# Kernel tuning notes

Measured on AMD Instinct MI355X. Metric: run time of the kernel, lower is better.

## Reference

```python
import jax, jax.numpy as jnp
import numpy as np

K_SIZE = 5


def extract_patches(x, k):
    # TF extract_image_patches with SAME zero padding, stride 1.
    # x: [B,H,W,C] -> [B,H,W,k*k,C], patch index ordered row-major over offsets.
    pad = k // 2
    B, H, W, C = x.shape
    xp = jnp.pad(x, ((0, 0), (pad, pad), (pad, pad), (0, 0)))
    slices = [xp[:, i:i + H, j:j + W, :] for i in range(k) for j in range(k)]
    return jnp.stack(slices, axis=3)  # [B,H,W,k*k,C]


def setup_inputs() -> dict:
    key = jax.random.key(0)
    k1, k2, k3, k4 = jax.random.split(key, 4)
    B, H, W, C, BIN = 4, 128, 128, 64, 64
    return {
        "main": jax.random.normal(k1, (B, H, W, C), jnp.float32),
        "main_value": jax.random.normal(k2, (B, H, W, BIN), jnp.float32),
        "ref": jax.random.normal(k3, (B, H, W, C), jnp.float32),
        "ref_value": jax.random.normal(k4, (B, H, W, BIN), jnp.float32),
    }


def reference(main, main_value, ref, ref_value):
    k = K_SIZE
    # local window keys: [B,H,W,k*k,C], then append main itself -> k*k+1 slots
    ref_stacked = extract_patches(ref, k)
    ref_main = jnp.concatenate([ref_stacked, main[:, :, :, None, :]], axis=-2)
    attn = jnp.einsum('bhwc,bhwkc->bhwk', main, ref_main)
    attn = jax.nn.softmax(attn, axis=-1)
    # values: [B,H,W,k*k+1,bin]
    ref_value_stacked = extract_patches(ref_value, k)
    ref_main_value = jnp.concatenate(
        [ref_value_stacked, main_value[:, :, :, None, :]], axis=-2)
    aggregation = jnp.einsum('bhwk,bhwki->bhwi', attn, ref_main_value)
    return aggregation
```

## Files before the change

### kernel.cpp

```cpp
#include <hip/hip_runtime.h>

#define BATCH 4
#define HH 128
#define WW 128
#define CC 64
#define PADR 2
#define NK 25
#define TH 8
#define TW 8
#define HALO 12
#define HPOS 144
#define LSTRIDE 68

__global__ __launch_bounds__(256) void local_attn_kernel(
    const float* __restrict__ main_,
    const float* __restrict__ main_value,
    const float* __restrict__ ref,
    const float* __restrict__ ref_value,
    float* __restrict__ out)
{
    __shared__ float buf[HPOS * LSTRIDE];

    const int t    = threadIdx.x;
    const int blk  = blockIdx.x;
    const int bx   = blk & 15;
    const int by   = (blk >> 4) & 15;
    const int b    = blk >> 8;

    const int lane = t & 63;
    const int wave = t >> 6;
    const int pxl  = lane >> 2;
    const int cg   = lane & 3;
    const int ly   = wave * 2 + (pxl >> 3);
    const int lx   = pxl & 7;
    const int gy   = by * TH + ly;
    const int gx   = bx * TW + lx;

    const size_t img_base = (size_t)b * HH * WW * CC;
    const size_t px_off   = img_base + ((size_t)gy * WW + gx) * CC + cg * 16;

    const int y0 = by * TH - PADR;
    const int x0 = bx * TW - PADR;

    {
        const int c4 = t & 15;
        int pos = t >> 4;
        #pragma unroll
        for (int it = 0; it < 9; ++it, pos += 16) {
            int hy = pos / 12, hx = pos - hy * 12;
            int yy = y0 + hy, xx = x0 + hx;
            float4 v = make_float4(0.f, 0.f, 0.f, 0.f);
            if ((unsigned)yy < HH && (unsigned)xx < WW)
                v = *(const float4*)(ref + img_base + ((size_t)yy * WW + xx) * CC + c4 * 4);
            *(float4*)(buf + pos * LSTRIDE + c4 * 4) = v;
        }
    }

    float q[16];
    #pragma unroll
    for (int i = 0; i < 4; ++i) {
        float4 v = *(const float4*)(main_ + px_off + i * 4);
        q[i*4+0] = v.x; q[i*4+1] = v.y; q[i*4+2] = v.z; q[i*4+3] = v.w;
    }

    __syncthreads();

    float p[26];
    #pragma unroll
    for (int k = 0; k < NK; ++k) {
        const int di = k / 5, dj = k % 5;
        const float* base = buf + ((ly + di) * 12 + (lx + dj)) * LSTRIDE + cg * 16;
        float acc = 0.f;
        #pragma unroll
        for (int i = 0; i < 4; ++i) {
            float4 v = *(const float4*)(base + i * 4);
            acc += q[i*4+0]*v.x + q[i*4+1]*v.y + q[i*4+2]*v.z + q[i*4+3]*v.w;
        }
        acc += __shfl_xor(acc, 1);
        acc += __shfl_xor(acc, 2);
        p[k] = acc;
    }
    {
        float acc = 0.f;
        #pragma unroll
        for (int c = 0; c < 16; ++c) acc += q[c] * q[c];
        acc += __shfl_xor(acc, 1);
        acc += __shfl_xor(acc, 2);
        p[25] = acc;
    }

    float m = p[0];
    #pragma unroll
    for (int k = 1; k < 26; ++k) m = fmaxf(m, p[k]);
    float s = 0.f;
    #pragma unroll
    for (int k = 0; k < 26; ++k) { p[k] = __expf(p[k] - m); s += p[k]; }
    const float rs = 1.f / s;

    __syncthreads();

    {
        const int c4 = t & 15;
        int pos = t >> 4;
        #pragma unroll
        for (int it = 0; it < 9; ++it, pos += 16) {
            int hy = pos / 12, hx = pos - hy * 12;
            int yy = y0 + hy, xx = x0 + hx;
            float4 v = make_float4(0.f, 0.f, 0.f, 0.f);
            if ((unsigned)yy < HH && (unsigned)xx < WW)
                v = *(const float4*)(ref_value + img_base + ((size_t)yy * WW + xx) * CC + c4 * 4);
            *(float4*)(buf + pos * LSTRIDE + c4 * 4) = v;
        }
    }
    __syncthreads();

    float acc[16];
    #pragma unroll
    for (int c = 0; c < 16; ++c) acc[c] = 0.f;

    #pragma unroll
    for (int k = 0; k < NK; ++k) {
        const int di = k / 5, dj = k % 5;
        const float* base = buf + ((ly + di) * 12 + (lx + dj)) * LSTRIDE + cg * 16;
        const float pk = p[k];
        #pragma unroll
        for (int i = 0; i < 4; ++i) {
            float4 v = *(const float4*)(base + i * 4);
            acc[i*4+0] += pk * v.x; acc[i*4+1] += pk * v.y;
            acc[i*4+2] += pk * v.z; acc[i*4+3] += pk * v.w;
        }
    }
    {
        const float pk = p[25];
        #pragma unroll
        for (int i = 0; i < 4; ++i) {
            float4 v = *(const float4*)(main_value + px_off + i * 4);
            acc[i*4+0] += pk * v.x; acc[i*4+1] += pk * v.y;
            acc[i*4+2] += pk * v.z; acc[i*4+3] += pk * v.w;
        }
    }

    #pragma unroll
    for (int i = 0; i < 4; ++i) {
        float4 v = make_float4(acc[i*4+0]*rs, acc[i*4+1]*rs,
                               acc[i*4+2]*rs, acc[i*4+3]*rs);
        *(float4*)(out + px_off + i * 4) = v;
    }
}

extern "C" void kernel_launch(void* const* d_in, const int* in_sizes, int n_in,
                              void* d_out, int out_size, void* d_ws, size_t ws_size,
                              hipStream_t stream) {
    const float* main_      = (const float*)d_in[0];
    const float* main_value = (const float*)d_in[1];
    const float* ref        = (const float*)d_in[2];
    const float* ref_value  = (const float*)d_in[3];
    float* out = (float*)d_out;

    local_attn_kernel<<<dim3(BATCH * 16 * 16), dim3(256), 0, stream>>>(
        main_, main_value, ref, ref_value, out);
}
```

Measured before the change: 29.90 us.

## Prefetch ref_value halo into registers early and remap blocks across XCDs

The ref_value halo tile is now loaded into registers at kernel start, together with the ref tile, so its global latency overlaps the QK dot products and softmax. After the second barrier those registers are written to shared memory, which avoids a second exposed global-load phase. Block indices are also permuted in groups of 8, likely to keep spatially adjacent tiles on the same XCD for L2 halo reuse, and launch bounds now request 4 blocks per CU. The cost is 36 extra VGPRs held live across the attention phase, which could cut occupancy or cause spills under the new launch-bounds limit.

```diff
diff --git a/kernel.cpp b/kernel.cpp
--- a/kernel.cpp
+++ b/kernel.cpp
@@ -12,7 +12,7 @@
 #define HPOS 144
 #define LSTRIDE 68
 
-__global__ __launch_bounds__(256) void local_attn_kernel(
+__global__ __launch_bounds__(256, 4) void local_attn_kernel(
     const float* __restrict__ main_,
     const float* __restrict__ main_value,
     const float* __restrict__ ref,
@@ -22,7 +22,9 @@
     __shared__ float buf[HPOS * LSTRIDE];
 
     const int t    = threadIdx.x;
-    const int blk  = blockIdx.x;
+    const int nwg  = BATCH * 16 * 16;
+    const int cpx  = nwg >> 3;
+    const int blk  = (blockIdx.x & 7) * cpx + (blockIdx.x >> 3);
     const int bx   = blk & 15;
     const int by   = (blk >> 4) & 15;
     const int b    = blk >> 8;
@@ -42,34 +44,54 @@
     const int y0 = by * TH - PADR;
     const int x0 = bx * TW - PADR;
 
-    {
-        const int c4 = t & 15;
-        int pos = t >> 4;
-        #pragma unroll
-        for (int it = 0; it < 9; ++it, pos += 16) {
-            int hy = pos / 12, hx = pos - hy * 12;
-            int yy = y0 + hy, xx = x0 + hx;
-            float4 v = make_float4(0.f, 0.f, 0.f, 0.f);
-            if ((unsigned)yy < HH && (unsigned)xx < WW)
-                v = *(const float4*)(ref + img_base + ((size_t)yy * WW + xx) * CC + c4 * 4);
-            *(float4*)(buf + pos * LSTRIDE + c4 * 4) = v;
-        }
+    const int c4   = t & 15;
+    const int pos0 = t >> 4;
+
+    float4 qv[4];
+    #pragma unroll
+    for (int i = 0; i < 4; ++i)
+        qv[i] = *(const float4*)(main_ + px_off + i * 4);
+
+    float4 kreg[9];
+    #pragma unroll
+    for (int it = 0; it < 9; ++it) {
+        int pos = pos0 + 16 * it;
+        int hy = pos / 12, hx = pos - hy * 12;
+        int yy = y0 + hy, xx = x0 + hx;
+        kreg[it] = make_float4(0.f, 0.f, 0.f, 0.f);
+        if ((unsigned)yy < HH && (unsigned)xx < WW)
+            kreg[it] = *(const float4*)(ref + img_base + ((size_t)yy * WW + xx) * CC + c4 * 4);
     }
+
+    float4 vstage[9];
+    #pragma unroll
+    for (int it = 0; it < 9; ++it) {
+        int pos = pos0 + 16 * it;
+        int hy = pos / 12, hx = pos - hy * 12;
+        int yy = y0 + hy, xx = x0 + hx;
+        vstage[it] = make_float4(0.f, 0.f, 0.f, 0.f);
+        if ((unsigned)yy < HH && (unsigned)xx < WW)
+            vstage[it] = *(const float4*)(ref_value + img_base + ((size_t)yy * WW + xx) * CC + c4 * 4);
+    }
+
+    #pragma unroll
+    for (int it = 0; it < 9; ++it)
+        *(float4*)(buf + (pos0 + 16 * it) * LSTRIDE + c4 * 4) = kreg[it];
+
+    __syncthreads();
 
     float q[16];
     #pragma unroll
     for (int i = 0; i < 4; ++i) {
-        float4 v = *(const float4*)(main_ + px_off + i * 4);
-        q[i*4+0] = v.x; q[i*4+1] = v.y; q[i*4+2] = v.z; q[i*4+3] = v.w;
+        q[i*4+0] = qv[i].x; q[i*4+1] = qv[i].y; q[i*4+2] = qv[i].z; q[i*4+3] = qv[i].w;
     }
 
-    __syncthreads();
-
     float p[26];
+    const float* mybase = buf + (ly * 12 + lx) * LSTRIDE + cg * 16;
     #pragma unroll
     for (int k = 0; k < NK; ++k) {
         const int di = k / 5, dj = k % 5;
-        const float* base = buf + ((ly + di) * 12 + (lx + dj)) * LSTRIDE + cg * 16;
+        const float* base = mybase + (di * 12 + dj) * LSTRIDE;
         float acc = 0.f;
         #pragma unroll
         for (int i = 0; i < 4; ++i) {
@@ -99,20 +121,16 @@
 
     __syncthreads();
 
-    {
-        const int c4 = t & 15;
-        int pos = t >> 4;
-        #pragma unroll
-        for (int it = 0; it < 9; ++it, pos += 16) {
-            int hy = pos / 12, hx = pos - hy * 12;
-            int yy = y0 + hy, xx = x0 + hx;
-            float4 v = make_float4(0.f, 0.f, 0.f, 0.f);
-            if ((unsigned)yy < HH && (unsigned)xx < WW)
-                v = *(const float4*)(ref_value + img_base + ((size_t)yy * WW + xx) * CC + c4 * 4);
-            *(float4*)(buf + pos * LSTRIDE + c4 * 4) = v;
-        }
-    }
+    #pragma unroll
+    for (int it = 0; it < 9; ++it)
+        *(float4*)(buf + (pos0 + 16 * it) * LSTRIDE + c4 * 4) = vstage[it];
+
     __syncthreads();
+
+    float4 mvv[4];
+    #pragma unroll
+    for (int i = 0; i < 4; ++i)
+        mvv[i] = *(const float4*)(main_value + px_off + i * 4);
 
     float acc[16];
     #pragma unroll
@@ -121,7 +139,7 @@
     #pragma unroll
     for (int k = 0; k < NK; ++k) {
         const int di = k / 5, dj = k % 5;
-        const float* base = buf + ((ly + di) * 12 + (lx + dj)) * LSTRIDE + cg * 16;
+        const float* base = mybase + (di * 12 + dj) * LSTRIDE;
         const float pk = p[k];
         #pragma unroll
         for (int i = 0; i < 4; ++i) {
@@ -134,9 +152,8 @@
         const float pk = p[25];
         #pragma unroll
         for (int i = 0; i < 4; ++i) {
-            float4 v = *(const float4*)(main_value + px_off + i * 4);
-            acc[i*4+0] += pk * v.x; acc[i*4+1] += pk * v.y;
-            acc[i*4+2] += pk * v.z; acc[i*4+3] += pk * v.w;
+            acc[i*4+0] += pk * mvv[i].x; acc[i*4+1] += pk * mvv[i].y;
+            acc[i*4+2] += pk * mvv[i].z; acc[i*4+3] += pk * mvv[i].w;
         }
     }
 
```

Result: faster. 26.98 us (-9.8%).
